# Kernel tuning notes

Hardware: AMD Instinct MI355X
Metric: run time of the kernel (lower is better)

## Reference

```python
import jax, jax.numpy as jnp
import numpy as np

BINS = 5
POINTS = 2
EPS_DIV = 1e-6
GN_GROUPS = 32
GN_EPS = 1e-5


def bilinear_sum(img, ys, xs):
    """Sum of bilinear samples with zero padding outside the image.
    img: (B, C, H, W); ys, xs: (B, K, H, W) absolute sample coords.
    Returns (B, C, H, W) = sum over K of bilinear(img, ys_k, xs_k)."""
    B, C, H, W = img.shape
    K = ys.shape[1]
    y0 = jnp.floor(ys)
    x0 = jnp.floor(xs)
    imgf = img.reshape(B, C, H * W)
    acc = jnp.zeros((B, C, K, H, W), img.dtype)
    for dy, dx in ((0, 0), (0, 1), (1, 0), (1, 1)):
        yi = y0 + dy
        xi = x0 + dx
        w = (1.0 - jnp.abs(ys - yi)) * (1.0 - jnp.abs(xs - xi))
        valid = (yi >= 0) & (yi <= H - 1) & (xi >= 0) & (xi <= W - 1)
        yc = jnp.clip(yi, 0, H - 1).astype(jnp.int32)
        xc = jnp.clip(xi, 0, W - 1).astype(jnp.int32)
        idx = (yc * W + xc).reshape(B, 1, K * H * W)
        g = jnp.take_along_axis(imgf, idx, axis=2).reshape(B, C, K, H, W)
        acc = acc + (w * valid.astype(img.dtype))[:, None] * g
    return acc.sum(axis=2)


def setup_inputs():
    key = jax.random.key(0)
    ks = jax.random.split(key, 6)
    B, C, H, W = 2, 256, 100, 152
    P, K = POINTS, BINS
    x = jax.random.normal(ks[0], (B, C, H, W), jnp.float32)
    offsets = jax.random.normal(ks[1], (B, P * K * 2, H, W), jnp.float32) * 2.0
    ef_w = jax.random.normal(ks[2], (P * C, C), jnp.float32) * 0.02
    ef_b = jnp.zeros((P * C,), jnp.float32)
    hm1_w = jax.random.normal(ks[3], (P, C, C), jnp.float32) * 0.02
    hm1_b = jnp.zeros((P, C), jnp.float32)
    hm2_w = jax.random.normal(ks[4], (P, C), jnp.float32) * 0.02
    hm2_b = jnp.zeros((P,), jnp.float32)
    merge_w = jax.random.normal(ks[5], (C, P * C), jnp.float32) * 0.02
    merge_b = jnp.zeros((C,), jnp.float32)
    gn_g = jnp.ones((C,), jnp.float32)
    gn_b = jnp.zeros((C,), jnp.float32)
    return {"x": x, "offsets": offsets, "ef_w": ef_w, "ef_b": ef_b,
            "hm1_w": hm1_w, "hm1_b": hm1_b, "hm2_w": hm2_w, "hm2_b": hm2_b,
            "merge_w": merge_w, "merge_b": merge_b, "gn_g": gn_g, "gn_b": gn_b}


def reference(x, offsets, ef_w, ef_b, hm1_w, hm1_b, hm2_w, hm2_b, merge_w, merge_b, gn_g, gn_b):
    B, C, H, W = x.shape
    P, K = POINTS, BINS
    # expand_feat: 1x1 conv C -> P*C
    ef = jnp.einsum('bchw,dc->bdhw', x, ef_w) + ef_b[None, :, None, None]
    efp = ef.reshape(B, P, C, H, W)
    # heatmap: grouped 1x1 conv (per-point) -> ReLU -> grouped 1x1 conv -> exp
    h = jax.nn.relu(jnp.einsum('bpchw,pdc->bpdhw', efp, hm1_w) + hm1_b[None, :, :, None, None])
    heat = jnp.exp(jnp.einsum('bpdhw,pd->bphw', h, hm2_w) + hm2_b[None, :, None, None])  # (B,P,H,W)
    # offsets: (B, P, K, 2, H, W) with channel layout [y, x] per bin.
    # base_offset cancels the [1,bins] kernel grid, so the deform conv with
    # all-ones weights is simply: sum over bins of bilinear samples at
    # (h + off_y, w + off_x).
    off = offsets.reshape(B, P, K, 2, H, W)
    hg = jnp.arange(H, dtype=x.dtype)[None, None, None, :, None]
    wg = jnp.arange(W, dtype=x.dtype)[None, None, None, None, :]
    ys = hg + off[:, :, :, 0]  # (B,P,K,H,W)
    xs = wg + off[:, :, :, 1]
    outs = []
    for p in range(P):
        # sample feat*heat (C channels) and heat (1 channel) together
        img = jnp.concatenate([efp[:, p] * heat[:, p][:, None], heat[:, p][:, None]], axis=1)
        s = bilinear_sum(img, ys[:, p], xs[:, p])  # (B, C+1, H, W)
        outs.append(s[:, :C] / (s[:, C:] + EPS_DIV))
    outs = jnp.concatenate(outs, axis=1)  # (B, P*C, H, W)
    merged = jnp.einsum('bchw,dc->bdhw', outs, merge_w) + merge_b[None, :, None, None]
    # GroupNorm(32, C) + ReLU
    g = merged.reshape(B, GN_GROUPS, C // GN_GROUPS, H, W)
    mu = g.mean(axis=(2, 3, 4), keepdims=True)
    var = g.var(axis=(2, 3, 4), keepdims=True)
    gn = ((g - mu) / jnp.sqrt(var + GN_EPS)).reshape(B, C, H, W)
    gn = gn * gn_g[None, :, None, None] + gn_b[None, :, None, None]
    return jax.nn.relu(gn)
```

## Files before the change

### kernel.cpp

```cpp
#include <hip/hip_runtime.h>

#define BINS 5
#define PTS  2
constexpr int Bx = 2, Cc = 256, Hh = 100, Ww = 152;
constexpr int HW = Hh * Ww;
constexpr int NTILE = 238;
constexpr float EPS_DIV = 1e-6f;
constexpr float GN_EPS  = 1e-5f;

typedef __attribute__((ext_vector_type(8)))  _Float16 hfrag;
typedef __attribute__((ext_vector_type(2)))  _Float16 h2;
typedef __attribute__((ext_vector_type(16))) float    f32x16;

__device__ __forceinline__ ushort f2h(float f) {
    return __builtin_bit_cast(ushort, (_Float16)f);
}
__device__ __forceinline__ float hlo(unsigned u) {
    return (float)__builtin_bit_cast(_Float16, (ushort)(u & 0xffffu));
}
__device__ __forceinline__ float hhi(unsigned u) {
    return (float)__builtin_bit_cast(_Float16, (ushort)(u >> 16));
}

#define GLL16(g, l) __builtin_amdgcn_global_load_lds( \
    (const __attribute__((address_space(1))) unsigned*)(g), \
    (__attribute__((address_space(3))) unsigned*)(l), 16, 0, 0)

#define MFMA32(a, b, c) __builtin_amdgcn_mfma_f32_32x32x16_f16(a, b, c, 0, 0, 0)

__global__ __launch_bounds__(256)
void k_pre(const float* __restrict__ efw, const float* __restrict__ w1,
           const float* __restrict__ mw, ushort* __restrict__ wb,
           const float* __restrict__ x, ushort* __restrict__ xbt)
{
    __shared__ float tile[32][33];
    const int bid = blockIdx.x;
    const int t = threadIdx.x;
    if (bid < 192) {
        int gid = bid * 256 + t;
        int i = gid * 8;
        int arr = i >> 17, off = i & 131071;
        const float* src = arr == 0 ? efw : (arr == 1 ? w1 : mw);
        float4 v0 = *(const float4*)(src + off);
        float4 v1 = *(const float4*)(src + off + 4);
        int outaddr;
        if (arr == 0) {
            int m = off >> 8, k = off & 255;
            outaddr = (((k >> 4) * 16 + (m >> 5)) * 64 + (m & 31) + 32 * ((k >> 3) & 1)) * 8;
        } else if (arr == 1) {
            int p = off >> 16, r = off & 65535;
            int m = r >> 8, k = r & 255;
            outaddr = p * 65536 +
                      (((k >> 4) * 8 + (m >> 5)) * 64 + (m & 31) + 32 * ((k >> 3) & 1)) * 8;
        } else {
            int m = off >> 9, k = off & 511;
            outaddr = (((k >> 4) * 8 + (m >> 5)) * 64 + (m & 31) + 32 * ((k >> 3) & 1)) * 8;
        }
        ushort o[8] = { f2h(v0.x), f2h(v0.y), f2h(v0.z), f2h(v0.w),
                        f2h(v1.x), f2h(v1.y), f2h(v1.z), f2h(v1.w) };
        *(uint4*)(wb + arr * 131072 + outaddr) = *(uint4*)o;
    } else {
        int r = bid - 192;
        const int b = r / 3800; r -= b * 3800;
        const int c0 = (r / 475) * 32;
        const int hw0 = (r % 475) * 32;
        const float* xb = x + ((size_t)b * Cc + c0) * HW + hw0;
        const int tx = t & 31, ty = t >> 5;
        #pragma unroll
        for (int rr = 0; rr < 4; rr++) {
            int c = ty + rr * 8;
            tile[c][tx] = xb[(size_t)c * HW + tx];
        }
        __syncthreads();
        const int hwl = t >> 3, c4 = (t & 7) * 4;
        ushort4 o = { f2h(tile[c4 + 0][hwl]), f2h(tile[c4 + 1][hwl]),
                      f2h(tile[c4 + 2][hwl]), f2h(tile[c4 + 3][hwl]) };
        *(ushort4*)&xbt[((size_t)b * HW + hw0 + hwl) * Cc + c0 + c4] = o;
    }
}

__global__ __launch_bounds__(512, 2)
void k_ef(const ushort* __restrict__ xbt, const ushort* __restrict__ wbe,
          const float* __restrict__ efb, ushort* __restrict__ efp)
{
    __shared__ ushort B0[64 * 256];
    __shared__ ushort B1[64 * 256];
    const int t = threadIdx.x;
    const int wv = t >> 6, ln = t & 63;
    const int l31 = ln & 31, lh = ln >> 5;
    const int b = blockIdx.y;
    const int tt0 = blockIdx.x * 2;
    const ushort* xb = xbt + (size_t)b * HW * Cc;

    hfrag A[2][16];
    #pragma unroll
    for (int mf = 0; mf < 2; mf++)
        #pragma unroll
        for (int ks = 0; ks < 16; ks++)
            A[mf][ks] = *(const hfrag*)&wbe[((ks * 16 + (wv * 2 + mf)) * 64 + ln) * 8];
    __builtin_amdgcn_sched_barrier(0);

    auto stageB = [&](int tt, ushort* dst) {
        int tp0 = tt * 64;
        #pragma unroll
        for (int j = 0; j < 4; j++) {
            int unit = j * 512 + t;
            int prow = unit >> 5, c8 = unit & 31;
            int pq = tp0 + prow; if (pq > HW - 1) pq = HW - 1;
            const ushort* g = xb + (size_t)pq * Cc + ((c8 ^ (prow & 7)) << 3);
            ushort* l = dst + (j * 512 + wv * 64) * 8;
            GLL16(g, l);
        }
    };
    stageB(tt0, B0);
    stageB(tt0 + 1, B1);
    __builtin_amdgcn_sched_barrier(0);
    asm volatile("s_waitcnt vmcnt(4)" ::: "memory");
    __builtin_amdgcn_s_barrier();
    __builtin_amdgcn_sched_barrier(0);

    auto compute = [&](int tt, const ushort* Bs) {
        f32x16 acc[2][2];
        #pragma unroll
        for (int mf = 0; mf < 2; mf++)
            #pragma unroll
            for (int pf = 0; pf < 2; pf++)
                #pragma unroll
                for (int r = 0; r < 16; r++) acc[mf][pf][r] = 0.f;
        #pragma unroll
        for (int ks = 0; ks < 16; ks++) {
            int c = ks * 2 + lh;
            #pragma unroll
            for (int pf = 0; pf < 2; pf++) {
                hfrag bf = *(const hfrag*)&Bs[(pf * 32 + l31) * 256 + ((c ^ (l31 & 7)) << 3)];
                acc[0][pf] = MFMA32(A[0][ks], bf, acc[0][pf]);
                acc[1][pf] = MFMA32(A[1][ks], bf, acc[1][pf]);
            }
        }
        const int tp0 = tt * 64;
        #pragma unroll
        for (int mf = 0; mf < 2; mf++) {
            int m0 = wv * 2 + mf;
            const int p_ = m0 >> 3;
            ushort* outb = efp + (size_t)((b * PTS + p_) * HW) * Cc;
            int chb = (m0 * 32) & 255;
            #pragma unroll
            for (int q = 0; q < 4; q++) {
                float4 bv = *(const float4*)&efb[m0 * 32 + q * 8 + 4 * lh];
                #pragma unroll
                for (int pf = 0; pf < 2; pf++) {
                    int px = tp0 + pf * 32 + l31;
                    if (px < HW) {
                        int ch = chb + q * 8 + 4 * lh;
                        ushort4 o = { f2h(acc[mf][pf][q * 4 + 0] + bv.x),
                                      f2h(acc[mf][pf][q * 4 + 1] + bv.y),
                                      f2h(acc[mf][pf][q * 4 + 2] + bv.z),
                                      f2h(acc[mf][pf][q * 4 + 3] + bv.w) };
                        *(ushort4*)&outb[(size_t)px * Cc + ch] = o;
                    }
                }
            }
        }
    };
    compute(tt0, B0);
    asm volatile("s_waitcnt vmcnt(0)" ::: "memory");
    __builtin_amdgcn_s_barrier();
    __builtin_amdgcn_sched_barrier(0);
    compute(tt0 + 1, B1);
}

__global__ __launch_bounds__(512, 2)
void k_heat(const ushort* __restrict__ efp, const ushort* __restrict__ wb1,
            const float* __restrict__ b1, const float* __restrict__ w2,
            const float* __restrict__ b2, float* __restrict__ heat)
{
    __shared__ ushort B0[64 * 256];
    __shared__ ushort B1[64 * 256];
    __shared__ float red[8][64];
    const int t = threadIdx.x;
    const int wv = t >> 6, ln = t & 63;
    const int l31 = ln & 31, lh = ln >> 5;
    const int zz = blockIdx.y;
    const int b = zz >> 1, p = zz & 1;
    const int tt0 = blockIdx.x * 2;
    const ushort* eb = efp + (size_t)((b * PTS + p) * HW) * Cc;
    const float* b1p = b1 + p * 256;
    const float* w2p = w2 + p * 256;
    const float b2v = b2[p];

    hfrag A[16];
    #pragma unroll
    for (int ks = 0; ks < 16; ks++)
        A[ks] = *(const hfrag*)&wb1[p * 65536 + ((ks * 8 + wv) * 64 + ln) * 8];
    __builtin_amdgcn_sched_barrier(0);

    auto stageB = [&](int tt, ushort* dst) {
        int tp0 = tt * 64;
        #pragma unroll
        for (int j = 0; j < 4; j++) {
            int unit = j * 512 + t;
            int prow = unit >> 5, c8 = unit & 31;
            int pq = tp0 + prow; if (pq > HW - 1) pq = HW - 1;
            const ushort* g = eb + (size_t)pq * Cc + ((c8 ^ (prow & 7)) << 3);
            ushort* l = dst + (j * 512 + wv * 64) * 8;
            GLL16(g, l);
        }
    };
    stageB(tt0, B0);
    stageB(tt0 + 1, B1);
    __builtin_amdgcn_sched_barrier(0);
    asm volatile("s_waitcnt vmcnt(4)" ::: "memory");
    __builtin_amdgcn_s_barrier();
    __builtin_amdgcn_sched_barrier(0);

    auto compute = [&](int tt, const ushort* Bs) {
        f32x16 acc[2];
        #pragma unroll
        for (int pf = 0; pf < 2; pf++)
            #pragma unroll
            for (int r = 0; r < 16; r++) acc[pf][r] = 0.f;
        #pragma unroll
        for (int ks = 0; ks < 16; ks++) {
            int c = ks * 2 + lh;
            #pragma unroll
            for (int pf = 0; pf < 2; pf++) {
                hfrag bf = *(const hfrag*)&Bs[(pf * 32 + l31) * 256 + ((c ^ (l31 & 7)) << 3)];
                acc[pf] = MFMA32(A[ks], bf, acc[pf]);
            }
        }
        float s[2] = {0.f, 0.f};
        #pragma unroll
        for (int q = 0; q < 4; q++) {
            float4 b1v = *(const float4*)&b1p[wv * 32 + q * 8 + 4 * lh];
            float4 w2v = *(const float4*)&w2p[wv * 32 + q * 8 + 4 * lh];
            #pragma unroll
            for (int pf = 0; pf < 2; pf++) {
                float h0 = acc[pf][q * 4 + 0] + b1v.x;
                float h1 = acc[pf][q * 4 + 1] + b1v.y;
                float h2_ = acc[pf][q * 4 + 2] + b1v.z;
                float h3 = acc[pf][q * 4 + 3] + b1v.w;
                s[pf] += w2v.x * (h0 > 0.f ? h0 : 0.f);
                s[pf] += w2v.y * (h1 > 0.f ? h1 : 0.f);
                s[pf] += w2v.z * (h2_ > 0.f ? h2_ : 0.f);
                s[pf] += w2v.w * (h3 > 0.f ? h3 : 0.f);
            }
        }
        s[0] += __shfl_xor(s[0], 32);
        s[1] += __shfl_xor(s[1], 32);
        if (lh == 0) {
            red[wv][l31]      = s[0];
            red[wv][32 + l31] = s[1];
        }
        asm volatile("s_waitcnt lgkmcnt(0)" ::: "memory");
        __builtin_amdgcn_s_barrier();
        if (t < 64) {
            float v = red[0][t] + red[1][t] + red[2][t] + red[3][t] +
                      red[4][t] + red[5][t] + red[6][t] + red[7][t];
            int px = tt * 64 + t;
            if (px < HW) heat[(size_t)(b * PTS + p) * HW + px] = expf(v + b2v);
        }
    };
    compute(tt0, B0);
    asm volatile("s_waitcnt vmcnt(0)" ::: "memory");
    __builtin_amdgcn_s_barrier();
    __builtin_amdgcn_sched_barrier(0);
    compute(tt0 + 1, B1);
}

__global__ __launch_bounds__(512, 2)
void k_sm(const ushort* __restrict__ efp, const float* __restrict__ heat,
          const float* __restrict__ offs, const ushort* __restrict__ wbm,
          const float* __restrict__ mb, ushort* __restrict__ mgb,
          float* __restrict__ part2)
{
    __shared__ ushort Bs[64 * 512];
    __shared__ uint2 s_wo[64][20];
    const int t = threadIdx.x;
    const int wv = t >> 6, ln = t & 63;
    const int l31 = ln & 31, lh = ln >> 5;
    const int bid = blockIdx.x;
    const int tile = (bid & 7) * 30 + (bid >> 3);
    if (tile >= NTILE) return;
    const int b = blockIdx.y;
    const int m0 = tile * 64;

    for (int p = 0; p < PTS; p++) {
        const float* heat_bp = heat + (size_t)(b * PTS + p) * HW;
        if (t < 64 * BINS) {
            int j = t / BINS, k = t - (t / BINS) * BINS;
            int hw = m0 + j;
            bool ok = hw < HW;
            int hwc = ok ? hw : HW - 1;
            int hh = hwc / Ww, ww = hwc - hh * Ww;
            int chy = (p * BINS + k) * 2;
            float oy = offs[((size_t)b * (PTS * BINS * 2) + chy)     * HW + hwc];
            float ox = offs[((size_t)b * (PTS * BINS * 2) + chy + 1) * HW + hwc];
            float ysf = (float)hh + oy;
            float xsf = (float)ww + ox;
            float y0 = floorf(ysf), x0 = floorf(xsf);
            #pragma unroll
            for (int dy = 0; dy < 2; dy++)
                #pragma unroll
                for (int dx = 0; dx < 2; dx++) {
                    float yi = y0 + dy, xi = x0 + dx;
                    float wgt = (1.f - fabsf(ysf - yi)) * (1.f - fabsf(xsf - xi));
                    bool valid = ok && (yi >= 0.f) && (yi <= (float)(Hh - 1)) &&
                                 (xi >= 0.f) && (xi <= (float)(Ww - 1));
                    int yc = (int)yi; yc = yc < 0 ? 0 : (yc > Hh - 1 ? Hh - 1 : yc);
                    int xc = (int)xi; xc = xc < 0 ? 0 : (xc > Ww - 1 ? Ww - 1 : xc);
                    int idx = yc * Ww + xc;
                    float wh = valid ? wgt * heat_bp[idx] : 0.f;
                    s_wo[j][k * 4 + dy * 2 + dx] =
                        make_uint2(__float_as_uint(wh), (unsigned)idx << 9);
                }
        }
        asm volatile("s_waitcnt lgkmcnt(0)" ::: "memory");
        __builtin_amdgcn_s_barrier();
        __builtin_amdgcn_sched_barrier(0);
        if (t < 64) {
            float s = 0.f;
            #pragma unroll
            for (int u = 0; u < 20; u++) s += __uint_as_float(s_wo[t][u].x);
            float inv = 1.f / (s + EPS_DIV);
            #pragma unroll
            for (int u = 0; u < 20; u++) {
                float w = __uint_as_float(s_wo[t][u].x) * inv;
                unsigned hw16 = (unsigned)f2h(w);
                s_wo[t][u].x = hw16 | (hw16 << 16);
            }
        }
        asm volatile("s_waitcnt lgkmcnt(0)" ::: "memory");
        __builtin_amdgcn_s_barrier();
        __builtin_amdgcn_sched_barrier(0);

        const int half = lh, c8 = l31;
        const char* efbase = (const char*)(efp + (size_t)((b * PTS + p) * HW) * Cc)
                             + c8 * 16;
        const int g = p * 32 + c8;
        #pragma unroll
        for (int i = 0; i < 8; i += 2) {
            const int j = wv * 8 + i + half;
            h2 a0 = (h2){0, 0}, a1 = (h2){0, 0}, a2 = (h2){0, 0}, a3 = (h2){0, 0};
            #pragma unroll
            for (int u = 0; u < 20; u++) {
                uint2 wo = s_wo[j][u];
                uint4 v = *(const uint4*)(efbase + wo.y);
                h2 wp = __builtin_bit_cast(h2, wo.x);
                a0 += wp * __builtin_bit_cast(h2, v.x);
                a1 += wp * __builtin_bit_cast(h2, v.y);
                a2 += wp * __builtin_bit_cast(h2, v.z);
                a3 += wp * __builtin_bit_cast(h2, v.w);
            }
            uint4 o = { __builtin_bit_cast(unsigned, a0), __builtin_bit_cast(unsigned, a1),
                        __builtin_bit_cast(unsigned, a2), __builtin_bit_cast(unsigned, a3) };
            *(uint4*)&Bs[j * 512 + ((g ^ (j & 7)) << 3)] = o;
        }
        asm volatile("s_waitcnt lgkmcnt(0)" ::: "memory");
        __builtin_amdgcn_s_barrier();
        __builtin_amdgcn_sched_barrier(0);
    }

    f32x16 acc[2];
    #pragma unroll
    for (int pf = 0; pf < 2; pf++)
        #pragma unroll
        for (int r = 0; r < 16; r++) acc[pf][r] = 0.f;
    #pragma unroll 1
    for (int c4 = 0; c4 < 4; c4++) {
        hfrag A8[8];
        #pragma unroll
        for (int k8 = 0; k8 < 8; k8++)
            A8[k8] = *(const hfrag*)&wbm[(((c4 * 8 + k8) * 8 + wv) * 64 + ln) * 8];
        #pragma unroll
        for (int k8 = 0; k8 < 8; k8++) {
            int c = (c4 * 8 + k8) * 2 + lh;
            #pragma unroll
            for (int pf = 0; pf < 2; pf++) {
                hfrag bf = *(const hfrag*)&Bs[(pf * 32 + l31) * 512 + ((c ^ (l31 & 7)) << 3)];
                acc[pf] = MFMA32(A8[k8], bf, acc[pf]);
            }
        }
    }

    float sg[4] = {0.f, 0.f, 0.f, 0.f};
    float qg[4] = {0.f, 0.f, 0.f, 0.f};
    #pragma unroll
    for (int q = 0; q < 4; q++) {
        float4 bv = *(const float4*)&mb[wv * 32 + q * 8 + 4 * lh];
        #pragma unroll
        for (int pf = 0; pf < 2; pf++) {
            int px = m0 + pf * 32 + l31;
            if (px < HW) {
                #pragma unroll
                for (int r = 0; r < 4; r++) {
                    float bb = r == 0 ? bv.x : (r == 1 ? bv.y : (r == 2 ? bv.z : bv.w));
                    float v = acc[pf][q * 4 + r] + bb;
                    int ch = wv * 32 + q * 8 + 4 * lh + r;
                    mgb[((size_t)b * Cc + ch) * HW + px] = f2h(v);
                    sg[q] += v; qg[q] += v * v;
                }
            }
        }
    }
    #pragma unroll
    for (int q = 0; q < 4; q++) {
        #pragma unroll
        for (int off = 1; off <= 32; off <<= 1) {
            sg[q] += __shfl_xor(sg[q], off);
            qg[q] += __shfl_xor(qg[q], off);
        }
    }
    if (ln == 0) {
        #pragma unroll
        for (int q = 0; q < 4; q++) {
            int g = wv * 4 + q;
            size_t idx = ((size_t)(b * 32 + g) * NTILE + tile) * 2;
            part2[idx + 0] = sg[q];
            part2[idx + 1] = qg[q];
        }
    }
}

__global__ __launch_bounds__(256)
void k_gnfinal(const float* __restrict__ part2, float* __restrict__ statf)
{
    const int bg = blockIdx.x;
    const int t = threadIdx.x;
    float s = 0.f, q = 0.f;
    if (t < NTILE) {
        s = part2[((size_t)bg * NTILE + t) * 2 + 0];
        q = part2[((size_t)bg * NTILE + t) * 2 + 1];
    }
    #pragma unroll
    for (int off = 1; off <= 32; off <<= 1) {
        s += __shfl_xor(s, off);
        q += __shfl_xor(q, off);
    }
    __shared__ float rs[4], rq[4];
    int wid = t >> 6;
    if ((t & 63) == 0) { rs[wid] = s; rq[wid] = q; }
    __syncthreads();
    if (t == 0) {
        float S = rs[0] + rs[1] + rs[2] + rs[3];
        float Q = rq[0] + rq[1] + rq[2] + rq[3];
        const float n = 8.f * HW;
        float mean = S / n;
        float var  = Q / n - mean * mean;
        statf[bg * 2 + 0] = mean;
        statf[bg * 2 + 1] = rsqrtf(var + GN_EPS);
    }
}

__global__ __launch_bounds__(256)
void k_gnapply(const ushort* __restrict__ mgb, const float* __restrict__ statf,
               const float* __restrict__ gg, const float* __restrict__ gb,
               float* __restrict__ out)
{
    const int i8 = blockIdx.x * 256 + threadIdx.x;
    const int i = i8 * 8;
    const int CHW = Cc * HW;
    const int b = i / CHW;
    const int r = i - b * CHW;
    const int c = r / HW;
    const int g = c >> 3;
    float mean = statf[(b * 32 + g) * 2 + 0];
    float istd = statf[(b * 32 + g) * 2 + 1];
    float sc = istd * gg[c];
    float sh = gb[c] - mean * sc;
    uint4 v = *(const uint4*)(mgb + i);
    float4 o0, o1;
    o0.x = fmaxf(hlo(v.x) * sc + sh, 0.f);
    o0.y = fmaxf(hhi(v.x) * sc + sh, 0.f);
    o0.z = fmaxf(hlo(v.y) * sc + sh, 0.f);
    o0.w = fmaxf(hhi(v.y) * sc + sh, 0.f);
    o1.x = fmaxf(hlo(v.z) * sc + sh, 0.f);
    o1.y = fmaxf(hhi(v.z) * sc + sh, 0.f);
    o1.z = fmaxf(hlo(v.w) * sc + sh, 0.f);
    o1.w = fmaxf(hhi(v.w) * sc + sh, 0.f);
    *(float4*)(out + i)     = o0;
    *(float4*)(out + i + 4) = o1;
}

extern "C" void kernel_launch(void* const* d_in, const int* in_sizes, int n_in,
                              void* d_out, int out_size, void* d_ws, size_t ws_size,
                              hipStream_t stream)
{
    const float* x    = (const float*)d_in[0];
    const float* offs = (const float*)d_in[1];
    const float* efw  = (const float*)d_in[2];
    const float* efb  = (const float*)d_in[3];
    const float* w1   = (const float*)d_in[4];
    const float* b1   = (const float*)d_in[5];
    const float* w2   = (const float*)d_in[6];
    const float* b2   = (const float*)d_in[7];
    const float* mw   = (const float*)d_in[8];
    const float* mb   = (const float*)d_in[9];
    const float* gg   = (const float*)d_in[10];
    const float* gb   = (const float*)d_in[11];
    float* out = (float*)d_out;

    ushort* wb    = (ushort*)d_ws;
    ushort* wbe   = wb;
    ushort* wb1   = wb + 131072;
    ushort* wbm   = wb + 262144;
    ushort* efp   = wb + 393216;
    ushort* outsb = efp + (size_t)Bx * PTS * HW * Cc;
    ushort* xbt   = outsb + (size_t)Bx * HW * PTS * Cc;
    ushort* mgb   = xbt + (size_t)Bx * HW * Cc;
    float*  heat  = (float*)(mgb + (size_t)Bx * Cc * HW);
    float*  part2 = heat + (size_t)Bx * PTS * HW;
    float*  statf = part2 + (size_t)64 * NTILE * 2;

    dim3 blk(256);
    k_pre    <<<dim3(7792),             blk, 0, stream>>>(efw, w1, mw, wb, x, xbt);
    k_ef     <<<dim3(119, Bx),    dim3(512), 0, stream>>>(xbt, wbe, efb, efp);
    k_heat   <<<dim3(119, 4),     dim3(512), 0, stream>>>(efp, wb1, b1, w2, b2, heat);
    k_sm     <<<dim3(240, Bx),    dim3(512), 0, stream>>>(efp, heat, offs, wbm, mb, mgb, part2);
    k_gnfinal<<<dim3(64),               blk, 0, stream>>>(part2, statf);
    k_gnapply<<<dim3(Bx * Cc * HW / 8 / 256), blk, 0, stream>>>(mgb, statf, gg, gb, out);
}
```

Before: 198.2 us.

## Halve sampling tile to 32 pixels and process both points concurrently across waves

The fused sample+merge kernel now handles 32 pixels per block instead of 64, which doubles the grid to 475 tiles per batch and remaps tiles onto XCDs. Both sampling points are set up and gathered in parallel by different waves, so the per-point loop and several barriers go away, and the merge GEMM does one MFMA stream per wave. The aim is more blocks and fewer serialized phases for better occupancy and latency hiding. The cost is reloading the merge weights per tile twice as often and more GroupNorm partials for the final reduction, which now loops over tiles.

```diff
diff --git a/kernel.cpp b/kernel.cpp
--- a/kernel.cpp
+++ b/kernel.cpp
@@ -4,7 +4,7 @@
 #define PTS  2
 constexpr int Bx = 2, Cc = 256, Hh = 100, Ww = 152;
 constexpr int HW = Hh * Ww;
-constexpr int NTILE = 238;
+constexpr int NTILE = 475;
 constexpr float EPS_DIV = 1e-6f;
 constexpr float GN_EPS  = 1e-5f;
 
@@ -273,77 +273,74 @@
           const float* __restrict__ mb, ushort* __restrict__ mgb,
           float* __restrict__ part2)
 {
-    __shared__ ushort Bs[64 * 512];
-    __shared__ uint2 s_wo[64][20];
+    __shared__ ushort Bs[32 * 512];
+    __shared__ uint2 s_wo[2][32][20];
     const int t = threadIdx.x;
     const int wv = t >> 6, ln = t & 63;
     const int l31 = ln & 31, lh = ln >> 5;
     const int bid = blockIdx.x;
-    const int tile = (bid & 7) * 30 + (bid >> 3);
-    if (tile >= NTILE) return;
+    const int xcd = bid & 7, ii = bid >> 3;
+    const int tile = (xcd < 3 ? xcd * 60 : 180 + (xcd - 3) * 59) + ii;
     const int b = blockIdx.y;
-    const int m0 = tile * 64;
-
-    for (int p = 0; p < PTS; p++) {
+    const int m0 = tile * 32;
+
+    if (t < 32 * BINS * PTS) {
+        int p = t / 160, r = t - p * 160;
+        int j = r / BINS, k = r - (r / BINS) * BINS;
+        int hw = m0 + j;
+        int hh = hw / Ww, ww = hw - hh * Ww;
         const float* heat_bp = heat + (size_t)(b * PTS + p) * HW;
-        if (t < 64 * BINS) {
-            int j = t / BINS, k = t - (t / BINS) * BINS;
-            int hw = m0 + j;
-            bool ok = hw < HW;
-            int hwc = ok ? hw : HW - 1;
-            int hh = hwc / Ww, ww = hwc - hh * Ww;
-            int chy = (p * BINS + k) * 2;
-            float oy = offs[((size_t)b * (PTS * BINS * 2) + chy)     * HW + hwc];
-            float ox = offs[((size_t)b * (PTS * BINS * 2) + chy + 1) * HW + hwc];
-            float ysf = (float)hh + oy;
-            float xsf = (float)ww + ox;
-            float y0 = floorf(ysf), x0 = floorf(xsf);
-            #pragma unroll
-            for (int dy = 0; dy < 2; dy++)
-                #pragma unroll
-                for (int dx = 0; dx < 2; dx++) {
-                    float yi = y0 + dy, xi = x0 + dx;
-                    float wgt = (1.f - fabsf(ysf - yi)) * (1.f - fabsf(xsf - xi));
-                    bool valid = ok && (yi >= 0.f) && (yi <= (float)(Hh - 1)) &&
-                                 (xi >= 0.f) && (xi <= (float)(Ww - 1));
-                    int yc = (int)yi; yc = yc < 0 ? 0 : (yc > Hh - 1 ? Hh - 1 : yc);
-                    int xc = (int)xi; xc = xc < 0 ? 0 : (xc > Ww - 1 ? Ww - 1 : xc);
-                    int idx = yc * Ww + xc;
-                    float wh = valid ? wgt * heat_bp[idx] : 0.f;
-                    s_wo[j][k * 4 + dy * 2 + dx] =
-                        make_uint2(__float_as_uint(wh), (unsigned)idx << 9);
-                }
-        }
-        asm volatile("s_waitcnt lgkmcnt(0)" ::: "memory");
-        __builtin_amdgcn_s_barrier();
-        __builtin_amdgcn_sched_barrier(0);
-        if (t < 64) {
-            float s = 0.f;
-            #pragma unroll
-            for (int u = 0; u < 20; u++) s += __uint_as_float(s_wo[t][u].x);
-            float inv = 1.f / (s + EPS_DIV);
+        int chy = (p * BINS + k) * 2;
+        float oy = offs[((size_t)b * (PTS * BINS * 2) + chy)     * HW + hw];
+        float ox = offs[((size_t)b * (PTS * BINS * 2) + chy + 1) * HW + hw];
+        float ysf = (float)hh + oy;
+        float xsf = (float)ww + ox;
+        float y0 = floorf(ysf), x0 = floorf(xsf);
+        #pragma unroll
+        for (int dy = 0; dy < 2; dy++)
+            #pragma unroll
+            for (int dx = 0; dx < 2; dx++) {
+                float yi = y0 + dy, xi = x0 + dx;
+                float wgt = (1.f - fabsf(ysf - yi)) * (1.f - fabsf(xsf - xi));
+                bool valid = (yi >= 0.f) && (yi <= (float)(Hh - 1)) &&
+                             (xi >= 0.f) && (xi <= (float)(Ww - 1));
+                int yc = (int)yi; yc = yc < 0 ? 0 : (yc > Hh - 1 ? Hh - 1 : yc);
+                int xc = (int)xi; xc = xc < 0 ? 0 : (xc > Ww - 1 ? Ww - 1 : xc);
+                int idx = yc * Ww + xc;
+                float wh = valid ? wgt * heat_bp[idx] : 0.f;
+                s_wo[p][j][k * 4 + dy * 2 + dx] =
+                    make_uint2(__float_as_uint(wh), (unsigned)idx << 9);
+            }
+    }
+    __syncthreads();
+    if (t < 64) {
+        int p = t >> 5, px = t & 31;
+        float s = 0.f;
+        #pragma unroll
+        for (int u = 0; u < 20; u++) s += __uint_as_float(s_wo[p][px][u].x);
+        float inv = 1.f / (s + EPS_DIV);
+        #pragma unroll
+        for (int u = 0; u < 20; u++) {
+            float w = __uint_as_float(s_wo[p][px][u].x) * inv;
+            unsigned hw16 = (unsigned)f2h(w);
+            s_wo[p][px][u].x = hw16 | (hw16 << 16);
+        }
+    }
+    __syncthreads();
+
+    {
+        const int p = wv >> 2;
+        const int jb = (wv & 3) * 8;
+        const int g = p * 32 + l31;
+        const char* efbase = (const char*)(efp + (size_t)((b * PTS + p) * HW) * Cc)
+                             + l31 * 16;
+        #pragma unroll
+        for (int i2 = 0; i2 < 8; i2 += 2) {
+            const int j = jb + i2 + lh;
+            h2 a0 = (h2){0, 0}, a1 = (h2){0, 0}, a2 = (h2){0, 0}, a3 = (h2){0, 0};
             #pragma unroll
             for (int u = 0; u < 20; u++) {
-                float w = __uint_as_float(s_wo[t][u].x) * inv;
-                unsigned hw16 = (unsigned)f2h(w);
-                s_wo[t][u].x = hw16 | (hw16 << 16);
-            }
-        }
-        asm volatile("s_waitcnt lgkmcnt(0)" ::: "memory");
-        __builtin_amdgcn_s_barrier();
-        __builtin_amdgcn_sched_barrier(0);
-
-        const int half = lh, c8 = l31;
-        const char* efbase = (const char*)(efp + (size_t)((b * PTS + p) * HW) * Cc)
-                             + c8 * 16;
-        const int g = p * 32 + c8;
-        #pragma unroll
-        for (int i = 0; i < 8; i += 2) {
-            const int j = wv * 8 + i + half;
-            h2 a0 = (h2){0, 0}, a1 = (h2){0, 0}, a2 = (h2){0, 0}, a3 = (h2){0, 0};
-            #pragma unroll
-            for (int u = 0; u < 20; u++) {
-                uint2 wo = s_wo[j][u];
+                uint2 wo = s_wo[p][j][u];
                 uint4 v = *(const uint4*)(efbase + wo.y);
                 h2 wp = __builtin_bit_cast(h2, wo.x);
                 a0 += wp * __builtin_bit_cast(h2, v.x);
@@ -353,18 +350,14 @@
             }
             uint4 o = { __builtin_bit_cast(unsigned, a0), __builtin_bit_cast(unsigned, a1),
                         __builtin_bit_cast(unsigned, a2), __builtin_bit_cast(unsigned, a3) };
-            *(uint4*)&Bs[j * 512 + ((g ^ (j & 7)) << 3)] = o;
-        }
-        asm volatile("s_waitcnt lgkmcnt(0)" ::: "memory");
-        __builtin_amdgcn_s_barrier();
-        __builtin_amdgcn_sched_barrier(0);
-    }
-
-    f32x16 acc[2];
+            *(uint4*)&Bs[j * 512 + ((g ^ j) << 3)] = o;
+        }
+    }
+    __syncthreads();
+
+    f32x16 acc;
     #pragma unroll
-    for (int pf = 0; pf < 2; pf++)
-        #pragma unroll
-        for (int r = 0; r < 16; r++) acc[pf][r] = 0.f;
+    for (int r = 0; r < 16; r++) acc[r] = 0.f;
     #pragma unroll 1
     for (int c4 = 0; c4 < 4; c4++) {
         hfrag A8[8];
@@ -374,32 +367,24 @@
         #pragma unroll
         for (int k8 = 0; k8 < 8; k8++) {
             int c = (c4 * 8 + k8) * 2 + lh;
-            #pragma unroll
-            for (int pf = 0; pf < 2; pf++) {
-                hfrag bf = *(const hfrag*)&Bs[(pf * 32 + l31) * 512 + ((c ^ (l31 & 7)) << 3)];
-                acc[pf] = MFMA32(A8[k8], bf, acc[pf]);
-            }
-        }
-    }
-
+            hfrag bf = *(const hfrag*)&Bs[l31 * 512 + ((c ^ l31) << 3)];
+            acc = MFMA32(A8[k8], bf, acc);
+        }
+    }
+
+    const int px = m0 + l31;
     float sg[4] = {0.f, 0.f, 0.f, 0.f};
     float qg[4] = {0.f, 0.f, 0.f, 0.f};
     #pragma unroll
     for (int q = 0; q < 4; q++) {
         float4 bv = *(const float4*)&mb[wv * 32 + q * 8 + 4 * lh];
         #pragma unroll
-        for (int pf = 0; pf < 2; pf++) {
-            int px = m0 + pf * 32 + l31;
-            if (px < HW) {
-                #pragma unroll
-                for (int r = 0; r < 4; r++) {
-                    float bb = r == 0 ? bv.x : (r == 1 ? bv.y : (r == 2 ? bv.z : bv.w));
-                    float v = acc[pf][q * 4 + r] + bb;
-                    int ch = wv * 32 + q * 8 + 4 * lh + r;
-                    mgb[((size_t)b * Cc + ch) * HW + px] = f2h(v);
-                    sg[q] += v; qg[q] += v * v;
-                }
-            }
+        for (int r = 0; r < 4; r++) {
+            float bb = r == 0 ? bv.x : (r == 1 ? bv.y : (r == 2 ? bv.z : bv.w));
+            float v = acc[q * 4 + r] + bb;
+            int ch = wv * 32 + q * 8 + 4 * lh + r;
+            mgb[((size_t)b * Cc + ch) * HW + px] = f2h(v);
+            sg[q] += v; qg[q] += v * v;
         }
     }
     #pragma unroll
@@ -427,9 +412,9 @@
     const int bg = blockIdx.x;
     const int t = threadIdx.x;
     float s = 0.f, q = 0.f;
-    if (t < NTILE) {
-        s = part2[((size_t)bg * NTILE + t) * 2 + 0];
-        q = part2[((size_t)bg * NTILE + t) * 2 + 1];
+    for (int u = t; u < NTILE; u += 256) {
+        s += part2[((size_t)bg * NTILE + u) * 2 + 0];
+        q += part2[((size_t)bg * NTILE + u) * 2 + 1];
     }
     #pragma unroll
     for (int off = 1; off <= 32; off <<= 1) {
@@ -504,8 +489,7 @@
     ushort* wb1   = wb + 131072;
     ushort* wbm   = wb + 262144;
     ushort* efp   = wb + 393216;
-    ushort* outsb = efp + (size_t)Bx * PTS * HW * Cc;
-    ushort* xbt   = outsb + (size_t)Bx * HW * PTS * Cc;
+    ushort* xbt   = efp + (size_t)Bx * PTS * HW * Cc;
     ushort* mgb   = xbt + (size_t)Bx * HW * Cc;
     float*  heat  = (float*)(mgb + (size_t)Bx * Cc * HW);
     float*  part2 = heat + (size_t)Bx * PTS * HW;
@@ -515,7 +499,7 @@
     k_pre    <<<dim3(7792),             blk, 0, stream>>>(efw, w1, mw, wb, x, xbt);
     k_ef     <<<dim3(119, Bx),    dim3(512), 0, stream>>>(xbt, wbe, efb, efp);
     k_heat   <<<dim3(119, 4),     dim3(512), 0, stream>>>(efp, wb1, b1, w2, b2, heat);
-    k_sm     <<<dim3(240, Bx),    dim3(512), 0, stream>>>(efp, heat, offs, wbm, mb, mgb, part2);
+    k_sm     <<<dim3(475, Bx),    dim3(512), 0, stream>>>(efp, heat, offs, wbm, mb, mgb, part2);
     k_gnfinal<<<dim3(64),               blk, 0, stream>>>(part2, statf);
     k_gnapply<<<dim3(Bx * Cc * HW / 8 / 256), blk, 0, stream>>>(mgb, statf, gg, gb, out);
 }
```

New measurement: 198.2 us. Within noise of the previous version (-0.0%).
